# Optimization experiments

Measured on AMD Instinct MI355X. Metric: run time of the kernel, lower is better.

## Reference

```python
import jax, jax.numpy as jnp
import numpy as np

N_NODE = 100_000
N_EDGE = 1_000_000
D = 64          # in_dim = out_dim
A = 64          # attn_dim
B = 8           # batchsize
N_REL = 200     # rel table size = 2*n_rel+1 = 401
N_ENT = 50_000
N_RELTAB = 2 * N_REL + 1


def setup_inputs() -> dict:
    key = jax.random.key(0)
    ks = jax.random.split(key, 16)
    # edges columns: [batch_query_idx, head_ent, rel, tail_ent, sub_local, obj_local]
    r_idx = jax.random.randint(ks[0], (N_EDGE,), 0, B)
    head = jax.random.randint(ks[1], (N_EDGE,), 0, N_ENT)
    rel = jax.random.randint(ks[2], (N_EDGE,), 0, N_RELTAB)
    tail = jax.random.randint(ks[3], (N_EDGE,), 0, N_ENT)
    sub = jax.random.randint(ks[4], (N_EDGE,), 0, N_NODE)
    obj = jax.random.randint(ks[5], (N_EDGE,), 0, N_NODE)
    edges = jnp.stack([r_idx, head, rel, tail, sub, obj], axis=1)
    nodes = jnp.stack([
        jax.random.randint(ks[6], (N_NODE,), 0, B),
        jax.random.randint(ks[7], (N_NODE,), 0, N_ENT)], axis=1)
    s = 1.0 / np.sqrt(D)
    return {
        "q_sub": jax.random.randint(ks[8], (B,), 0, N_ENT),
        "q_rel": jax.random.randint(ks[9], (B,), 0, N_RELTAB),
        "hidden": jax.random.normal(ks[10], (N_NODE, D), jnp.float32),
        "edges": edges,
        "nodes": nodes,
        "old_nodes_new_idx": jax.random.randint(ks[11], (50_000,), 0, N_NODE),
        "batchsize": B,
        "rel_emb": jax.random.normal(ks[12], (N_RELTAB, D), jnp.float32) * s,
        "Ws": jax.random.normal(ks[13], (A, D), jnp.float32) * s,
        "Wr": jax.random.normal(ks[14], (A, D), jnp.float32) * s,
        "Wqr_w": jax.random.normal(ks[15], (A, D), jnp.float32) * s,
        "Wqr_b": jnp.zeros((A,), jnp.float32),
        "walpha_w": jax.random.normal(jax.random.fold_in(key, 101), (1, A), jnp.float32) * (1.0 / np.sqrt(A)),
        "walpha_b": jnp.zeros((1,), jnp.float32),
        "Wh": jax.random.normal(jax.random.fold_in(key, 102), (D, D), jnp.float32) * s,
    }


def reference(q_sub, q_rel, hidden, edges, nodes, old_nodes_new_idx, batchsize,
              rel_emb, Ws, Wr, Wqr_w, Wqr_b, walpha_w, walpha_b, Wh):
    sub = edges[:, 4]   # local source node index [E]
    rel = edges[:, 2]   # relation index        [E]
    obj = edges[:, 5]   # local target node     [E]
    r_idx = edges[:, 0]  # which query each edge belongs to [E]

    hs = hidden[sub]                 # [E, D] gather of node hidden states
    hr = rel_emb[rel]                # [E, D] relation embedding (rela_embed(h, r) = rel_emb[r])
    h_qr = rel_emb[q_rel][r_idx]     # [E, D] query relation embedding per edge

    # attention MLP: sigmoid(w_alpha @ relu(Ws hs + Wr hr + Wqr h_qr + b))
    pre = (jnp.einsum('ed,ad->ea', hs, Ws)
           + jnp.einsum('ed,ad->ea', hr, Wr)
           + jnp.einsum('ed,ad->ea', h_qr, Wqr_w) + Wqr_b)        # [E, A]
    alpha = jax.nn.sigmoid(jnp.einsum('ea,oa->eo', jax.nn.relu(pre), walpha_w) + walpha_b)  # [E, 1]

    message = alpha * (hs + hr)      # [E, D]
    n_node = hidden.shape[0]
    message_agg = jax.ops.segment_sum(message, obj, num_segments=n_node)  # [N, D]
    hidden_new = jnp.einsum('nd,od->no', message_agg, Wh)  # act = identity
    return hidden_new
```

## Files before the change

### kernel.cpp

```cpp
#include <hip/hip_runtime.h>
#include <hip/hip_fp16.h>
#include <cstdint>
#include <cstddef>

#define DD 64
#define N_RELTAB 401
#define N_QR 8
#define T_ROWS (N_RELTAB + N_QR)
#define WPB 4

__global__ __launch_bounds__(64) void build_C(
    const float* __restrict__ rel_emb, const float* __restrict__ Wr,
    const float* __restrict__ Wqr_w, const float* __restrict__ Wqr_b,
    const int* __restrict__ q_rel, float* __restrict__ Cf)
{
    int r = blockIdx.x, a = threadIdx.x;
    const float* w; const float* src; float acc;
    if (r < N_RELTAB) { w = Wr + a * DD; src = rel_emb + r * DD; acc = 0.f; }
    else {
        int k = r - N_RELTAB;
        w = Wqr_w + a * DD;
        src = rel_emb + q_rel[k] * DD;
        acc = Wqr_b[a];
    }
#pragma unroll
    for (int d = 0; d < DD; ++d) acc = fmaf(src[d], w[d], acc);
    Cf[r * DD + a] = acc;
}

__global__ __launch_bounds__(256) void rowmat(
    const float* __restrict__ in, const float* __restrict__ W,
    float* __restrict__ out, int nrows)
{
    int n = blockIdx.x * 256 + threadIdx.x;
    if (n >= nrows) return;
    float row[DD];
    const float4* rp = (const float4*)(in + ((size_t)n << 6));
#pragma unroll
    for (int j = 0; j < DD / 4; ++j) {
        float4 v = rp[j];
        row[4*j+0] = v.x; row[4*j+1] = v.y; row[4*j+2] = v.z; row[4*j+3] = v.w;
    }
    float4* op = (float4*)(out + ((size_t)n << 6));
    for (int a0 = 0; a0 < DD; a0 += 4) {
        const float* w0 = W + a0 * DD;
        float s0 = 0.f, s1 = 0.f, s2 = 0.f, s3 = 0.f;
#pragma unroll
        for (int d = 0; d < DD; ++d) {
            float r = row[d];
            s0 = fmaf(w0[d],          r, s0);
            s1 = fmaf(w0[DD + d],     r, s1);
            s2 = fmaf(w0[2 * DD + d], r, s2);
            s3 = fmaf(w0[3 * DD + d], r, s3);
        }
        float4 o; o.x = s0; o.y = s1; o.z = s2; o.w = s3;
        op[a0 >> 2] = o;
    }
}

__global__ __launch_bounds__(256) void hist_kernel(
    const int* __restrict__ edges, int* __restrict__ counts, int n_edge)
{
    int e = blockIdx.x * 256 + threadIdx.x;
    if (e < n_edge) atomicAdd(&counts[edges[6 * e + 5]], 1);
}

__global__ __launch_bounds__(1024) void scan1(
    const int* __restrict__ counts, int* __restrict__ offsets,
    int* __restrict__ bsums, int n)
{
    __shared__ int wsum[16];
    int t = threadIdx.x, i = blockIdx.x * 1024 + t;
    int lane = t & 63, wid = t >> 6;
    int c = (i < n) ? counts[i] : 0;
    int v = c;
#pragma unroll
    for (int d = 1; d < 64; d <<= 1) { int u = __shfl_up(v, d); if (lane >= d) v += u; }
    if (lane == 63) wsum[wid] = v;
    __syncthreads();
    if (wid == 0) {
        int s = (lane < 16) ? wsum[lane] : 0;
#pragma unroll
        for (int d = 1; d < 16; d <<= 1) { int u = __shfl_up(s, d); if (lane >= d) s += u; }
        if (lane < 16) wsum[lane] = s;
    }
    __syncthreads();
    int woff = (wid == 0) ? 0 : wsum[wid - 1];
    if (i < n) offsets[i] = woff + v - c;
    if (t == 1023) bsums[blockIdx.x] = wsum[15];
}

__global__ __launch_bounds__(1024) void scan_small(
    const int* __restrict__ bsums, int* __restrict__ boffs, int nb)
{
    __shared__ int wsum[16];
    int t = threadIdx.x, lane = t & 63, wid = t >> 6;
    int c = (t < nb) ? bsums[t] : 0;
    int v = c;
#pragma unroll
    for (int d = 1; d < 64; d <<= 1) { int u = __shfl_up(v, d); if (lane >= d) v += u; }
    if (lane == 63) wsum[wid] = v;
    __syncthreads();
    if (wid == 0) {
        int s = (lane < 16) ? wsum[lane] : 0;
#pragma unroll
        for (int d = 1; d < 16; d <<= 1) { int u = __shfl_up(s, d); if (lane >= d) s += u; }
        if (lane < 16) wsum[lane] = s;
    }
    __syncthreads();
    int woff = (wid == 0) ? 0 : wsum[wid - 1];
    if (t < nb) boffs[t] = woff + v - c;
}

__global__ __launch_bounds__(1024) void scan3(
    int* __restrict__ offsets, int* __restrict__ cursor,
    const int* __restrict__ boffs, int n)
{
    int i = blockIdx.x * 1024 + threadIdx.x;
    if (i < n) {
        int v = offsets[i] + boffs[blockIdx.x];
        offsets[i] = v;
        cursor[i] = v;
    }
}

__global__ __launch_bounds__(256) void build_sorted(
    const int* __restrict__ edges, int* __restrict__ cursor,
    uint64_t* __restrict__ sorted, int n_edge)
{
    int e = blockIdx.x * 256 + threadIdx.x;
    if (e >= n_edge) return;
    const int2* ep = (const int2*)(edges + 6 * e);
    int ridx = ep[0].x;
    int rel  = ep[1].x;
    int2 so  = ep[2];
    int pos = atomicAdd(&cursor[so.y], 1);
    uint32_t pay = (uint32_t)so.x | ((uint32_t)rel << 17) | ((uint32_t)ridx << 26);
    sorted[pos] = (uint64_t)pay | ((uint64_t)(uint32_t)so.y << 32);
}

__global__ __launch_bounds__(64 * WPB) void fused_aggregate(
    const uint64_t* __restrict__ sorted, const float* __restrict__ X,
    const float* __restrict__ hidden, const float* __restrict__ Cf,
    const float* __restrict__ rel_emb, const float* __restrict__ walpha_w,
    const float* __restrict__ walpha_b, float* __restrict__ agg,
    int n_edge, int n_node)
{
    __shared__ float sQ[N_QR * DD];
    __shared__ uint2 hdr[WPB][DD];
    __shared__ __half sS[WPB][DD][DD + 2];
    int tid = threadIdx.x;
    int lane = tid & 63, wid = tid >> 6;
    for (int i = tid; i < N_QR * DD; i += 64 * WPB) sQ[i] = Cf[N_RELTAB * DD + i];

    long wchunk = (long)blockIdx.x * WPB + wid;
    long e = wchunk * DD + lane;
    uint64_t p = (e < n_edge) ? sorted[e]
                              : ((uint64_t)(uint32_t)n_node << 32);
    hdr[wid][lane] = make_uint2((uint32_t)p, (uint32_t)(p >> 32));
    __syncthreads();

    float wa = walpha_w[lane];
    float wb = walpha_b[0];

#pragma unroll 4
    for (int j = 0; j < DD; ++j) {
        uint32_t pj = __builtin_amdgcn_readfirstlane(hdr[wid][j].x);
        int sub  = (int)(pj & 0x1FFFFu);
        int rel  = (int)((pj >> 17) & 0x1FFu);
        int ridx = (int)((pj >> 26) & 7u);
        float x = X[((size_t)sub << 6) + lane];
        float c = Cf[(rel << 6) + lane];
        float q = sQ[(ridx << 6) + lane];
        sS[wid][j][lane] = __float2half(fmaxf(x + c + q, 0.f) * wa);
    }
    __syncthreads();

    float t = 0.f;
    const __half2* row2 = (const __half2*)&sS[wid][lane][0];
#pragma unroll
    for (int a2 = 0; a2 < DD / 2; ++a2) {
        float2 f = __half22float2(row2[a2]);
        t += f.x + f.y;
    }
    float alpha_l = 1.f / (1.f + __expf(-(t + wb)));

    float acc = 0.f;
    int prev = (int)__builtin_amdgcn_readfirstlane(hdr[wid][0].y);
    bool firstseg = true;
    for (int j = 0; j < DD; ++j) {
        uint32_t pj = __builtin_amdgcn_readfirstlane(hdr[wid][j].x);
        int oj      = (int)__builtin_amdgcn_readfirstlane(hdr[wid][j].y);
        if (oj != prev) {
            if (prev < n_node) {
                if (firstseg) atomicAdd(&agg[((size_t)prev << 6) + lane], acc);
                else          agg[((size_t)prev << 6) + lane] = acc;
            }
            firstseg = false;
            acc = 0.f;
            prev = oj;
        }
        if (oj < n_node) {
            int sub = (int)(pj & 0x1FFFFu);
            int rel = (int)((pj >> 17) & 0x1FFu);
            float h = hidden[((size_t)sub << 6) + lane];
            float r = rel_emb[(rel << 6) + lane];
            float aj = __uint_as_float(__builtin_amdgcn_readlane(__float_as_uint(alpha_l), j));
            acc = fmaf(aj, h + r, acc);
        }
    }
    if (prev < n_node) atomicAdd(&agg[((size_t)prev << 6) + lane], acc);
}

extern "C" void kernel_launch(void* const* d_in, const int* in_sizes, int n_in,
                              void* d_out, int out_size, void* d_ws, size_t ws_size,
                              hipStream_t stream)
{
    const int*   q_rel    = (const int*)d_in[1];
    const float* hidden   = (const float*)d_in[2];
    const int*   edges    = (const int*)d_in[3];
    const float* rel_emb  = (const float*)d_in[7];
    const float* Ws       = (const float*)d_in[8];
    const float* Wr       = (const float*)d_in[9];
    const float* Wqr_w    = (const float*)d_in[10];
    const float* Wqr_b    = (const float*)d_in[11];
    const float* walpha_w = (const float*)d_in[12];
    const float* walpha_b = (const float*)d_in[13];
    const float* Wh       = (const float*)d_in[14];
    float* out = (float*)d_out;

    const int n_node = in_sizes[2] / DD;
    const int n_edge = in_sizes[3] / 6;
    const int NB = (n_node + 1023) / 1024;

    char* w = (char*)d_ws;
    float*    X       = (float*)w;     w += (size_t)n_node * DD * 4;
    float*    agg     = (float*)w;     w += (size_t)n_node * DD * 4;
    uint64_t* sorted  = (uint64_t*)w;  w += (size_t)n_edge * 8;
    int*      counts  = (int*)w;       w += (size_t)n_node * 4;
    int*      offsets = (int*)w;       w += (size_t)n_node * 4;
    int*      cursor  = (int*)w;       w += (size_t)n_node * 4;
    int*      bsums   = (int*)w;       w += 4096;
    int*      boffs   = (int*)w;       w += 4096;
    float*    Cf      = (float*)w;     w += (size_t)T_ROWS * DD * 4;

    build_C<<<T_ROWS, 64, 0, stream>>>(rel_emb, Wr, Wqr_w, Wqr_b, q_rel, Cf);
    rowmat<<<(n_node + 255) / 256, 256, 0, stream>>>(hidden, Ws, X, n_node);
    hipMemsetAsync(counts, 0, (size_t)n_node * 4, stream);
    hipMemsetAsync(agg, 0, (size_t)n_node * DD * 4, stream);
    hist_kernel<<<(n_edge + 255) / 256, 256, 0, stream>>>(edges, counts, n_edge);
    scan1<<<NB, 1024, 0, stream>>>(counts, offsets, bsums, n_node);
    scan_small<<<1, 1024, 0, stream>>>(bsums, boffs, NB);
    scan3<<<NB, 1024, 0, stream>>>(offsets, cursor, boffs, n_node);
    build_sorted<<<(n_edge + 255) / 256, 256, 0, stream>>>(edges, cursor, sorted, n_edge);
    const int nwaves = (n_edge + DD - 1) / DD;
    fused_aggregate<<<(nwaves + WPB - 1) / WPB, 64 * WPB, 0, stream>>>(
        sorted, X, hidden, Cf, rel_emb, walpha_w, walpha_b, agg, n_edge, n_node);
    rowmat<<<(n_node + 255) / 256, 256, 0, stream>>>(agg, Wh, out, n_node);
}
```

Baseline: 460.5 us.

## Tile rowmat via LDS, store X in bf16, pack edge keys early, shrink chunks

The row-matmul kernel now stages 64-row tiles in shared memory and has 256 threads compute them cooperatively. The projection X is stored as bf16 to halve gather traffic in the aggregate kernel. The histogram pass also emits packed edge keys, so the scatter pass reads 8-byte keys instead of the strided edge rows. The fused aggregate now works on 32-edge chunks, reading payloads from registers via readlane instead of shared headers, and adds a launch-bounds occupancy hint. The cost is an extra key buffer, bf16 rounding of the attention pre-activations, and roughly double the number of boundary atomics.

```diff
diff --git a/kernel.cpp b/kernel.cpp
--- a/kernel.cpp
+++ b/kernel.cpp
@@ -7,7 +7,17 @@
 #define N_RELTAB 401
 #define N_QR 8
 #define T_ROWS (N_RELTAB + N_QR)
+#define CHUNK 32
 #define WPB 4
+
+__device__ __forceinline__ uint16_t f2bf(float f) {
+    uint32_t u = __float_as_uint(f);
+    u += 0x7fffu + ((u >> 16) & 1u);
+    return (uint16_t)(u >> 16);
+}
+__device__ __forceinline__ float bf2f(uint16_t u) {
+    return __uint_as_float(((uint32_t)u) << 16);
+}
 
 __global__ __launch_bounds__(64) void build_C(
     const float* __restrict__ rel_emb, const float* __restrict__ Wr,
@@ -28,105 +38,83 @@
     Cf[r * DD + a] = acc;
 }
 
-__global__ __launch_bounds__(256) void rowmat(
+template<bool BF16OUT>
+__global__ __launch_bounds__(256) void rowmat_t(
     const float* __restrict__ in, const float* __restrict__ W,
-    float* __restrict__ out, int nrows)
-{
-    int n = blockIdx.x * 256 + threadIdx.x;
-    if (n >= nrows) return;
-    float row[DD];
-    const float4* rp = (const float4*)(in + ((size_t)n << 6));
-#pragma unroll
-    for (int j = 0; j < DD / 4; ++j) {
-        float4 v = rp[j];
-        row[4*j+0] = v.x; row[4*j+1] = v.y; row[4*j+2] = v.z; row[4*j+3] = v.w;
-    }
-    float4* op = (float4*)(out + ((size_t)n << 6));
-    for (int a0 = 0; a0 < DD; a0 += 4) {
-        const float* w0 = W + a0 * DD;
-        float s0 = 0.f, s1 = 0.f, s2 = 0.f, s3 = 0.f;
-#pragma unroll
-        for (int d = 0; d < DD; ++d) {
-            float r = row[d];
-            s0 = fmaf(w0[d],          r, s0);
-            s1 = fmaf(w0[DD + d],     r, s1);
-            s2 = fmaf(w0[2 * DD + d], r, s2);
-            s3 = fmaf(w0[3 * DD + d], r, s3);
-        }
-        float4 o; o.x = s0; o.y = s1; o.z = s2; o.w = s3;
-        op[a0 >> 2] = o;
-    }
-}
-
-__global__ __launch_bounds__(256) void hist_kernel(
-    const int* __restrict__ edges, int* __restrict__ counts, int n_edge)
-{
-    int e = blockIdx.x * 256 + threadIdx.x;
-    if (e < n_edge) atomicAdd(&counts[edges[6 * e + 5]], 1);
-}
-
-__global__ __launch_bounds__(1024) void scan1(
-    const int* __restrict__ counts, int* __restrict__ offsets,
-    int* __restrict__ bsums, int n)
-{
-    __shared__ int wsum[16];
-    int t = threadIdx.x, i = blockIdx.x * 1024 + t;
-    int lane = t & 63, wid = t >> 6;
-    int c = (i < n) ? counts[i] : 0;
-    int v = c;
-#pragma unroll
-    for (int d = 1; d < 64; d <<= 1) { int u = __shfl_up(v, d); if (lane >= d) v += u; }
-    if (lane == 63) wsum[wid] = v;
-    __syncthreads();
-    if (wid == 0) {
-        int s = (lane < 16) ? wsum[lane] : 0;
-#pragma unroll
-        for (int d = 1; d < 16; d <<= 1) { int u = __shfl_up(s, d); if (lane >= d) s += u; }
-        if (lane < 16) wsum[lane] = s;
-    }
-    __syncthreads();
-    int woff = (wid == 0) ? 0 : wsum[wid - 1];
-    if (i < n) offsets[i] = woff + v - c;
-    if (t == 1023) bsums[blockIdx.x] = wsum[15];
-}
-
-__global__ __launch_bounds__(1024) void scan_small(
-    const int* __restrict__ bsums, int* __restrict__ boffs, int nb)
-{
-    __shared__ int wsum[16];
-    int t = threadIdx.x, lane = t & 63, wid = t >> 6;
-    int c = (t < nb) ? bsums[t] : 0;
-    int v = c;
-#pragma unroll
-    for (int d = 1; d < 64; d <<= 1) { int u = __shfl_up(v, d); if (lane >= d) v += u; }
-    if (lane == 63) wsum[wid] = v;
-    __syncthreads();
-    if (wid == 0) {
-        int s = (lane < 16) ? wsum[lane] : 0;
-#pragma unroll
-        for (int d = 1; d < 16; d <<= 1) { int u = __shfl_up(s, d); if (lane >= d) s += u; }
-        if (lane < 16) wsum[lane] = s;
-    }
-    __syncthreads();
-    int woff = (wid == 0) ? 0 : wsum[wid - 1];
-    if (t < nb) boffs[t] = woff + v - c;
-}
-
-__global__ __launch_bounds__(1024) void scan3(
-    int* __restrict__ offsets, int* __restrict__ cursor,
-    const int* __restrict__ boffs, int n)
-{
-    int i = blockIdx.x * 1024 + threadIdx.x;
-    if (i < n) {
-        int v = offsets[i] + boffs[blockIdx.x];
-        offsets[i] = v;
-        cursor[i] = v;
-    }
-}
-
-__global__ __launch_bounds__(256) void build_sorted(
-    const int* __restrict__ edges, int* __restrict__ cursor,
-    uint64_t* __restrict__ sorted, int n_edge)
+    void* __restrict__ outv, int nrows)
+{
+    __shared__ float sIn[DD][DD + 1];
+    int r0 = blockIdx.x * DD;
+    int t = threadIdx.x;
+    int vr = nrows - r0; if (vr > DD) vr = DD;
+
+    const float4* gin = (const float4*)(in + (size_t)r0 * DD);
+    int vf4 = vr * (DD / 4);
+#pragma unroll
+    for (int k = 0; k < 4; ++k) {
+        int f = t + k * 256;
+        float4 v = (f < vf4) ? gin[f] : make_float4(0.f, 0.f, 0.f, 0.f);
+        int row = f >> 4, c4 = (f & 15) * 4;
+        sIn[row][c4] = v.x; sIn[row][c4+1] = v.y; sIn[row][c4+2] = v.z; sIn[row][c4+3] = v.w;
+    }
+    __syncthreads();
+
+    int row = t & 63, q = t >> 6;
+    float acc[16];
+#pragma unroll
+    for (int c = 0; c < 16; ++c) acc[c] = 0.f;
+    const float* wq = W + (q * 16) * DD;
+    for (int d4 = 0; d4 < 16; ++d4) {
+        float a0 = sIn[row][4*d4+0], a1 = sIn[row][4*d4+1];
+        float a2 = sIn[row][4*d4+2], a3 = sIn[row][4*d4+3];
+#pragma unroll
+        for (int c = 0; c < 16; ++c) {
+            const float* wr = wq + c * DD + d4 * 4;
+            acc[c] = fmaf(a0, wr[0], acc[c]);
+            acc[c] = fmaf(a1, wr[1], acc[c]);
+            acc[c] = fmaf(a2, wr[2], acc[c]);
+            acc[c] = fmaf(a3, wr[3], acc[c]);
+        }
+    }
+    __syncthreads();
+
+    if (BF16OUT) {
+        uint32_t (*sOutU)[33] = (uint32_t (*)[33])&sIn[0][0];
+#pragma unroll
+        for (int c2 = 0; c2 < 8; ++c2)
+            sOutU[row][q * 8 + c2] =
+                (uint32_t)f2bf(acc[2*c2]) | ((uint32_t)f2bf(acc[2*c2+1]) << 16);
+        __syncthreads();
+        uint32_t* outU = (uint32_t*)outv;
+        int vu = vr * (DD / 2);
+#pragma unroll
+        for (int k = 0; k < 8; ++k) {
+            int u = t + k * 256;
+            if (u < vu) outU[(size_t)r0 * (DD / 2) + u] = sOutU[u >> 5][u & 31];
+        }
+    } else {
+#pragma unroll
+        for (int c = 0; c < 16; ++c) sIn[row][q * 16 + c] = acc[c];
+        __syncthreads();
+        float4* out4 = (float4*)outv;
+        int vf = vr * (DD / 4);
+#pragma unroll
+        for (int k = 0; k < 4; ++k) {
+            int f = t + k * 256;
+            if (f < vf) {
+                int rr = f >> 4, c4 = (f & 15) * 4;
+                float4 v;
+                v.x = sIn[rr][c4]; v.y = sIn[rr][c4+1];
+                v.z = sIn[rr][c4+2]; v.w = sIn[rr][c4+3];
+                out4[(size_t)r0 * (DD / 4) + f] = v;
+            }
+        }
+    }
+}
+
+__global__ __launch_bounds__(256) void hist_emit(
+    const int* __restrict__ edges, int* __restrict__ counts,
+    uint64_t* __restrict__ keys, int n_edge)
 {
     int e = blockIdx.x * 256 + threadIdx.x;
     if (e >= n_edge) return;
@@ -134,78 +122,153 @@
     int ridx = ep[0].x;
     int rel  = ep[1].x;
     int2 so  = ep[2];
-    int pos = atomicAdd(&cursor[so.y], 1);
+    atomicAdd(&counts[so.y], 1);
     uint32_t pay = (uint32_t)so.x | ((uint32_t)rel << 17) | ((uint32_t)ridx << 26);
-    sorted[pos] = (uint64_t)pay | ((uint64_t)(uint32_t)so.y << 32);
-}
-
-__global__ __launch_bounds__(64 * WPB) void fused_aggregate(
-    const uint64_t* __restrict__ sorted, const float* __restrict__ X,
+    keys[e] = (uint64_t)pay | ((uint64_t)(uint32_t)so.y << 32);
+}
+
+__global__ __launch_bounds__(1024) void scan1(
+    const int* __restrict__ counts, int* __restrict__ offsets,
+    int* __restrict__ bsums, int n)
+{
+    __shared__ int wsum[16];
+    int t = threadIdx.x, i = blockIdx.x * 1024 + t;
+    int lane = t & 63, wid = t >> 6;
+    int c = (i < n) ? counts[i] : 0;
+    int v = c;
+#pragma unroll
+    for (int d = 1; d < 64; d <<= 1) { int u = __shfl_up(v, d); if (lane >= d) v += u; }
+    if (lane == 63) wsum[wid] = v;
+    __syncthreads();
+    if (wid == 0) {
+        int s = (lane < 16) ? wsum[lane] : 0;
+#pragma unroll
+        for (int d = 1; d < 16; d <<= 1) { int u = __shfl_up(s, d); if (lane >= d) s += u; }
+        if (lane < 16) wsum[lane] = s;
+    }
+    __syncthreads();
+    int woff = (wid == 0) ? 0 : wsum[wid - 1];
+    if (i < n) offsets[i] = woff + v - c;
+    if (t == 1023) bsums[blockIdx.x] = wsum[15];
+}
+
+__global__ __launch_bounds__(1024) void scan_small(
+    const int* __restrict__ bsums, int* __restrict__ boffs, int nb)
+{
+    __shared__ int wsum[16];
+    int t = threadIdx.x, lane = t & 63, wid = t >> 6;
+    int c = (t < nb) ? bsums[t] : 0;
+    int v = c;
+#pragma unroll
+    for (int d = 1; d < 64; d <<= 1) { int u = __shfl_up(v, d); if (lane >= d) v += u; }
+    if (lane == 63) wsum[wid] = v;
+    __syncthreads();
+    if (wid == 0) {
+        int s = (lane < 16) ? wsum[lane] : 0;
+#pragma unroll
+        for (int d = 1; d < 16; d <<= 1) { int u = __shfl_up(s, d); if (lane >= d) s += u; }
+        if (lane < 16) wsum[lane] = s;
+    }
+    __syncthreads();
+    int woff = (wid == 0) ? 0 : wsum[wid - 1];
+    if (t < nb) boffs[t] = woff + v - c;
+}
+
+__global__ __launch_bounds__(1024) void scan3(
+    int* __restrict__ offsets, int* __restrict__ cursor,
+    const int* __restrict__ boffs, int n)
+{
+    int i = blockIdx.x * 1024 + threadIdx.x;
+    if (i < n) {
+        int v = offsets[i] + boffs[blockIdx.x];
+        offsets[i] = v;
+        cursor[i] = v;
+    }
+}
+
+__global__ __launch_bounds__(256) void build_sorted(
+    const uint64_t* __restrict__ keys, int* __restrict__ cursor,
+    uint64_t* __restrict__ sorted, int n_edge)
+{
+    int e = blockIdx.x * 256 + threadIdx.x;
+    if (e >= n_edge) return;
+    uint64_t k = keys[e];
+    int obj = (int)(k >> 32);
+    int pos = atomicAdd(&cursor[obj], 1);
+    sorted[pos] = k;
+}
+
+__global__ __launch_bounds__(256, 4) void fused_aggregate(
+    const uint64_t* __restrict__ sorted, const uint16_t* __restrict__ Xb,
     const float* __restrict__ hidden, const float* __restrict__ Cf,
     const float* __restrict__ rel_emb, const float* __restrict__ walpha_w,
     const float* __restrict__ walpha_b, float* __restrict__ agg,
     int n_edge, int n_node)
 {
     __shared__ float sQ[N_QR * DD];
-    __shared__ uint2 hdr[WPB][DD];
-    __shared__ __half sS[WPB][DD][DD + 2];
-    int tid = threadIdx.x;
-    int lane = tid & 63, wid = tid >> 6;
+    __shared__ __half sS[WPB][CHUNK][DD + 2];
+    int tid = threadIdx.x, lane = tid & 63, wid = tid >> 6;
     for (int i = tid; i < N_QR * DD; i += 64 * WPB) sQ[i] = Cf[N_RELTAB * DD + i];
-
-    long wchunk = (long)blockIdx.x * WPB + wid;
-    long e = wchunk * DD + lane;
-    uint64_t p = (e < n_edge) ? sorted[e]
-                              : ((uint64_t)(uint32_t)n_node << 32);
-    hdr[wid][lane] = make_uint2((uint32_t)p, (uint32_t)(p >> 32));
-    __syncthreads();
+    __syncthreads();
+
+    long chunk = (long)blockIdx.x * WPB + wid;
+    long base = chunk * CHUNK;
+    if (base >= n_edge) return;
+
+    int e_l = (int)base + (lane & 31);
+    uint64_t k = (lane < 32 && e_l < n_edge)
+                     ? sorted[e_l]
+                     : ((uint64_t)(uint32_t)n_node << 32);
+    uint32_t pay = (uint32_t)k;
+    int obj      = (int)(k >> 32);
 
     float wa = walpha_w[lane];
     float wb = walpha_b[0];
 
-#pragma unroll 4
-    for (int j = 0; j < DD; ++j) {
-        uint32_t pj = __builtin_amdgcn_readfirstlane(hdr[wid][j].x);
+#pragma unroll 8
+    for (int j = 0; j < CHUNK; ++j) {
+        uint32_t pj = (uint32_t)__builtin_amdgcn_readlane((int)pay, j);
         int sub  = (int)(pj & 0x1FFFFu);
         int rel  = (int)((pj >> 17) & 0x1FFu);
         int ridx = (int)((pj >> 26) & 7u);
-        float x = X[((size_t)sub << 6) + lane];
+        float x = bf2f(Xb[((size_t)sub << 6) + lane]);
         float c = Cf[(rel << 6) + lane];
         float q = sQ[(ridx << 6) + lane];
         sS[wid][j][lane] = __float2half(fmaxf(x + c + q, 0.f) * wa);
     }
-    __syncthreads();
-
-    float t = 0.f;
-    const __half2* row2 = (const __half2*)&sS[wid][lane][0];
-#pragma unroll
-    for (int a2 = 0; a2 < DD / 2; ++a2) {
+
+    int eb = lane & 31, hb = lane >> 5;
+    const __half2* row2 = (const __half2*)&sS[wid][eb][hb * 32];
+    float tsum = 0.f;
+#pragma unroll
+    for (int a2 = 0; a2 < 16; ++a2) {
         float2 f = __half22float2(row2[a2]);
-        t += f.x + f.y;
-    }
-    float alpha_l = 1.f / (1.f + __expf(-(t + wb)));
+        tsum += f.x + f.y;
+    }
+    tsum += __shfl_xor(tsum, 32);
+    float alpha = 1.f / (1.f + __expf(-(tsum + wb)));
 
     float acc = 0.f;
-    int prev = (int)__builtin_amdgcn_readfirstlane(hdr[wid][0].y);
-    bool firstseg = true;
-    for (int j = 0; j < DD; ++j) {
-        uint32_t pj = __builtin_amdgcn_readfirstlane(hdr[wid][j].x);
-        int oj      = (int)__builtin_amdgcn_readfirstlane(hdr[wid][j].y);
+    int prev = __builtin_amdgcn_readlane(obj, 0);
+    bool first = true;
+#pragma unroll 4
+    for (int j = 0; j < CHUNK; ++j) {
+        int oj = __builtin_amdgcn_readlane(obj, j);
         if (oj != prev) {
             if (prev < n_node) {
-                if (firstseg) atomicAdd(&agg[((size_t)prev << 6) + lane], acc);
-                else          agg[((size_t)prev << 6) + lane] = acc;
+                float* dst = &agg[((size_t)prev << 6) + lane];
+                if (first) atomicAdd(dst, acc); else *dst = acc;
             }
-            firstseg = false;
-            acc = 0.f;
-            prev = oj;
+            first = false; acc = 0.f; prev = oj;
         }
         if (oj < n_node) {
+            uint32_t pj = (uint32_t)__builtin_amdgcn_readlane((int)pay, j);
             int sub = (int)(pj & 0x1FFFFu);
             int rel = (int)((pj >> 17) & 0x1FFu);
             float h = hidden[((size_t)sub << 6) + lane];
             float r = rel_emb[(rel << 6) + lane];
-            float aj = __uint_as_float(__builtin_amdgcn_readlane(__float_as_uint(alpha_l), j));
+            float aj = __uint_as_float(
+                (uint32_t)__builtin_amdgcn_readlane((int)__float_as_uint(alpha), j));
             acc = fmaf(aj, h + r, acc);
         }
     }
@@ -234,9 +297,10 @@
     const int NB = (n_node + 1023) / 1024;
 
     char* w = (char*)d_ws;
-    float*    X       = (float*)w;     w += (size_t)n_node * DD * 4;
+    uint16_t* Xb      = (uint16_t*)w;  w += (size_t)n_node * DD * 2;
     float*    agg     = (float*)w;     w += (size_t)n_node * DD * 4;
     uint64_t* sorted  = (uint64_t*)w;  w += (size_t)n_edge * 8;
+    uint64_t* keys    = (uint64_t*)w;  w += (size_t)n_edge * 8;
     int*      counts  = (int*)w;       w += (size_t)n_node * 4;
     int*      offsets = (int*)w;       w += (size_t)n_node * 4;
     int*      cursor  = (int*)w;       w += (size_t)n_node * 4;
@@ -245,16 +309,16 @@
     float*    Cf      = (float*)w;     w += (size_t)T_ROWS * DD * 4;
 
     build_C<<<T_ROWS, 64, 0, stream>>>(rel_emb, Wr, Wqr_w, Wqr_b, q_rel, Cf);
-    rowmat<<<(n_node + 255) / 256, 256, 0, stream>>>(hidden, Ws, X, n_node);
+    rowmat_t<true><<<(n_node + DD - 1) / DD, 256, 0, stream>>>(hidden, Ws, Xb, n_node);
     hipMemsetAsync(counts, 0, (size_t)n_node * 4, stream);
     hipMemsetAsync(agg, 0, (size_t)n_node * DD * 4, stream);
-    hist_kernel<<<(n_edge + 255) / 256, 256, 0, stream>>>(edges, counts, n_edge);
+    hist_emit<<<(n_edge + 255) / 256, 256, 0, stream>>>(edges, counts, keys, n_edge);
     scan1<<<NB, 1024, 0, stream>>>(counts, offsets, bsums, n_node);
     scan_small<<<1, 1024, 0, stream>>>(bsums, boffs, NB);
     scan3<<<NB, 1024, 0, stream>>>(offsets, cursor, boffs, n_node);
-    build_sorted<<<(n_edge + 255) / 256, 256, 0, stream>>>(edges, cursor, sorted, n_edge);
-    const int nwaves = (n_edge + DD - 1) / DD;
-    fused_aggregate<<<(nwaves + WPB - 1) / WPB, 64 * WPB, 0, stream>>>(
-        sorted, X, hidden, Cf, rel_emb, walpha_w, walpha_b, agg, n_edge, n_node);
-    rowmat<<<(n_node + 255) / 256, 256, 0, stream>>>(agg, Wh, out, n_node);
-}
+    build_sorted<<<(n_edge + 255) / 256, 256, 0, stream>>>(keys, cursor, sorted, n_edge);
+    const int nchunks = (n_edge + CHUNK - 1) / CHUNK;
+    fused_aggregate<<<(nchunks + WPB - 1) / WPB, 64 * WPB, 0, stream>>>(
+        sorted, Xb, hidden, Cf, rel_emb, walpha_w, walpha_b, agg, n_edge, n_node);
+    rowmat_t<false><<<(n_node + DD - 1) / DD, 256, 0, stream>>>(agg, Wh, out, n_node);
+}
```

New measurement: 428.3 us. -7.0%, faster.
